# Kernel optimization log

Hardware: AMD Instinct MI355X
Metric: run time of the kernel (lower is better)

The kernel has to match this reference:

```python
import jax, jax.numpy as jnp
import numpy as np

HID = 1024   # hidden_dim
H = 16       # num_head
D = 64       # head_dim
W = 64       # window_size (one-sided attention radius)


def setup_inputs() -> dict:
    key = jax.random.key(0)
    ks = jax.random.split(key, 10)
    B, S = 2, 4096
    s = 0.02
    X = jax.random.normal(ks[0], (B, S, HID), jnp.float32)
    mask = jnp.ones((B, S), jnp.float32)
    Wq = jax.random.normal(ks[1], (HID, H * D), jnp.float32) * s
    bq = jnp.zeros((H * D,), jnp.float32)
    Wk = jax.random.normal(ks[2], (HID, H * D), jnp.float32) * s
    bk = jnp.zeros((H * D,), jnp.float32)
    Wv = jax.random.normal(ks[3], (HID, H * D), jnp.float32) * s
    bv = jnp.zeros((H * D,), jnp.float32)
    Wo = jax.random.normal(ks[4], (H * D, HID), jnp.float32) * s
    bo = jnp.zeros((HID,), jnp.float32)
    return dict(X=X, mask=mask, Wq=Wq, bq=bq, Wk=Wk, bk=bk, Wv=Wv, bv=bv, Wo=Wo, bo=bo)


def _chunk3(T, nC):
    # T: [B,H,S,D] -> [B,H,nC,3W,D]: for chunk c, keys of chunks c-1, c, c+1 (zero-padded at ends)
    B, Hh, S, Dd = T.shape
    Tp = jnp.pad(T, ((0, 0), (0, 0), (W, W), (0, 0))).reshape(B, Hh, nC + 2, W, Dd)
    return jnp.concatenate([Tp[:, :, :-2], Tp[:, :, 1:-1], Tp[:, :, 2:]], axis=3)


def reference(X, mask, Wq, bq, Wk, bk, Wv, bv, Wo, bo):
    B, S0, _ = X.shape
    pad = W - S0 % W  # matches torch: always >= 1 (full window if divisible)
    Xp = jnp.pad(X, ((0, 0), (0, pad), (0, 0)))
    mp = jnp.pad(mask, ((0, 0), (0, pad)))  # padded keys masked out
    S = S0 + pad
    nC = S // W

    def proj(Wm, b):
        return (Xp @ Wm + b).reshape(B, S, H, D).transpose(0, 2, 1, 3)  # [B,H,S,D]

    Q, K, V = proj(Wq, bq), proj(Wk, bk), proj(Wv, bv)
    Qc = Q.reshape(B, H, nC, W, D)
    K3 = _chunk3(K, nC)
    V3 = _chunk3(V, nC)

    # banded scores: query i attends keys j with |i - j| <= W
    scores = jnp.einsum('bhcqd,bhckd->bhcqk', Qc, K3) / jnp.asarray(np.sqrt(D), jnp.float32)
    qi = jnp.arange(W)[:, None]
    kj = jnp.arange(3 * W)[None, :]
    band = (kj >= qi) & (kj <= qi + 2 * W)  # [W, 3W]
    m3 = jnp.pad(mp, ((0, 0), (W, W))).reshape(B, nC + 2, W)
    m3 = jnp.concatenate([m3[:, :-2], m3[:, 1:-1], m3[:, 2:]], axis=2)  # [B,nC,3W]
    valid = band[None, None, None, :, :] & (m3[:, None, :, None, :] > 0)
    scores = jnp.where(valid, scores, -1e9)
    A = jax.nn.softmax(scores, axis=-1)
    ctx = jnp.einsum('bhcqk,bhckd->bhcqd', A, V3).reshape(B, H, S, D)
    out = ctx.transpose(0, 2, 1, 3).reshape(B, S, H * D) @ Wo + bo
    return out[:, :S0]
```

## Files before the change

kernel.cpp:

```cpp
#include <hip/hip_runtime.h>

typedef unsigned short u16;
typedef unsigned int u32;
typedef __bf16 bf16x8 __attribute__((ext_vector_type(8)));
typedef u16 u16x8 __attribute__((ext_vector_type(8)));
typedef float floatx4 __attribute__((ext_vector_type(4)));

#define MFMA16(a, b, c) __builtin_amdgcn_mfma_f32_16x16x32_bf16((a), (b), (c), 0, 0, 0)

#define B_ 2
#define S0 4096
#define NH 16
#define HD 64
#define HID 1024

__device__ __forceinline__ float bf2f(u16 u) {
  union { u32 i; float f; } x; x.i = ((u32)u) << 16; return x.f;
}
__device__ __forceinline__ u16 f2bf(float f) {
  union { float f; u32 i; } x; x.f = f;
  u32 r = x.i + 0x7FFFu + ((x.i >> 16) & 1u);
  return (u16)(r >> 16);
}

__device__ __forceinline__ void glds16(const u16* g, u16* l) {
  __builtin_amdgcn_global_load_lds(
      (const __attribute__((address_space(1))) u32*)g,
      (__attribute__((address_space(3))) u32*)l, 16, 0, 0);
}

__global__ __launch_bounds__(256) void prep(
    const float* __restrict__ X, const float* __restrict__ mask,
    const float* __restrict__ Wq, const float* __restrict__ bq,
    const float* __restrict__ Wk, const float* __restrict__ bk,
    const float* __restrict__ Wv, const float* __restrict__ bv,
    const float* __restrict__ Wo, const float* __restrict__ bo,
    u16* __restrict__ cX, u16* __restrict__ cmask, u16* __restrict__ cb,
    u16* __restrict__ WqkvT, u16* __restrict__ WoT) {
  __shared__ u16 tile[64][66];
  int bid = blockIdx.x;
  if (bid < 4096) {
    int i = (bid * 256 + threadIdx.x) * 8;
    const float4* Xv = (const float4*)(X + i);
    float4 a = Xv[0], b = Xv[1];
    u16x8 v;
    v[0] = f2bf(a.x); v[1] = f2bf(a.y); v[2] = f2bf(a.z); v[3] = f2bf(a.w);
    v[4] = f2bf(b.x); v[5] = f2bf(b.y); v[6] = f2bf(b.z); v[7] = f2bf(b.w);
    *(u16x8*)(cX + i) = v;
  } else if (bid < 4144) {
    int tid = (bid - 4096) * 256 + threadIdx.x;
    if (tid < B_ * S0) {
      cmask[tid] = f2bf(mask[tid]);
    } else {
      int j = tid - B_ * S0;
      int seg = j >> 10, idx = j & 1023;
      const float* src = (seg == 0) ? bq : (seg == 1) ? bk : (seg == 2) ? bv : bo;
      cb[seg * 1024 + idx] = f2bf(src[idx]);
    }
  } else {
    int idx = bid - 4144;
    int mat = idx >> 8;
    const float* src = (mat == 0) ? Wq : (mat == 1) ? Wk : (mat == 2) ? Wv : Wo;
    u16* dst = (mat < 3) ? (WqkvT + (size_t)mat * HID * HID) : WoT;
    int t0 = ((idx >> 4) & 15) * 64;
    int c0 = (idx & 15) * 64;
    int tx = threadIdx.x & 63, ty = threadIdx.x >> 6;
#pragma unroll
    for (int i = 0; i < 16; i++) {
      int r = i * 4 + ty;
      tile[r][tx] = f2bf(src[(size_t)(t0 + r) * HID + c0 + tx]);
    }
    __syncthreads();
#pragma unroll
    for (int i = 0; i < 16; i++) {
      int r = i * 4 + ty;
      dst[(size_t)(c0 + r) * HID + t0 + tx] = tile[tx][r];
    }
  }
}

template <int BN, int MODE, int NMAJOR, int SWZ>
__global__ __launch_bounds__(256) void gemm_bf16_tn(
    const u16* __restrict__ A, const u16* __restrict__ Bt,
    const u16* __restrict__ cb, void* __restrict__ outp, int K) {
  constexpr int NT = BN / 32;
  __shared__ alignas(16) u16 sA[128 * 64];
  __shared__ alignas(16) u16 sB[BN * 64];
  int t = threadIdx.x;
  int wave = t >> 6, lane = t & 63;
  int wm = wave >> 1, wn = wave & 1;
  int quad = lane >> 4, l16 = lane & 15;
  int tile_m, tile_n;
  if (SWZ) {
    int lin = blockIdx.y * gridDim.x + blockIdx.x;
    int wg = (lin & 7) * 256 + (lin >> 3);
    tile_m = (wg >> 5) * 128;
    tile_n = (wg & 31) * BN;
  } else {
    tile_m = (NMAJOR ? blockIdx.y : blockIdx.x) * 128;
    tile_n = (NMAJOR ? blockIdx.x : blockIdx.y) * BN;
  }

  floatx4 acc[4][NT] = {};

  int row_l = lane >> 3;
  int col_l = ((lane & 7) ^ row_l) * 8;
  const u16* Ag = A + (size_t)(tile_m + wave * 8 + row_l) * K + col_l;
  const u16* Bg = Bt + (size_t)(tile_n + wave * 8 + row_l) * K + col_l;
  u16* lA = sA + wave * 8 * 64;
  u16* lB = sB + wave * 8 * 64;

  for (int k0 = 0; k0 < K; k0 += 64) {
    __syncthreads();
#pragma unroll
    for (int r = 0; r < 4; r++)
      glds16(Ag + (size_t)(r * 32) * K + k0, lA + r * 2048);
#pragma unroll
    for (int r = 0; r < BN / 32; r++)
      glds16(Bg + (size_t)(r * 32) * K + k0, lB + r * 2048);
    __syncthreads();

#pragma unroll
    for (int ks = 0; ks < 2; ks++) {
      bf16x8 af[4], bfr[NT];
#pragma unroll
      for (int mt = 0; mt < 4; mt++) {
        int row = wm * 64 + mt * 16 + l16;
        int p = (ks * 4 + quad) ^ (row & 7);
        af[mt] = *(const bf16x8*)(sA + row * 64 + p * 8);
      }
#pragma unroll
      for (int nt = 0; nt < NT; nt++) {
        int row = wn * (BN / 2) + nt * 16 + l16;
        int p = (ks * 4 + quad) ^ (row & 7);
        bfr[nt] = *(const bf16x8*)(sB + row * 64 + p * 8);
      }
#pragma unroll
      for (int mt = 0; mt < 4; mt++)
#pragma unroll
        for (int nt = 0; nt < NT; nt++)
          acc[mt][nt] = MFMA16(af[mt], bfr[nt], acc[mt][nt]);
    }
  }

  if (MODE == 0) {
    u16* op = (u16*)outp;
#pragma unroll
    for (int mt = 0; mt < 4; mt++) {
      int row0 = tile_m + wm * 64 + mt * 16 + quad * 4;
      int bb = row0 >> 12;
      int sbase = row0 & (S0 - 1);
#pragma unroll
      for (int nt = 0; nt < NT; nt++) {
        int col = tile_n + wn * (BN / 2) + nt * 16 + l16;
        int p = col >> 10;
        int rem = col & 1023;
        float bias = bf2f(cb[p * 1024 + rem]);
        int hh = rem >> 6, dd = rem & 63;
        u16* dp = op + ((size_t)(((p * 2 + bb) * NH + hh)) * S0 + sbase) * HD + dd;
#pragma unroll
        for (int r = 0; r < 4; r++)
          dp[(size_t)r * HD] = f2bf(acc[mt][nt][r] + bias);
      }
    }
  } else {
    float* op = (float*)outp;
#pragma unroll
    for (int mt = 0; mt < 4; mt++) {
      int row0 = tile_m + wm * 64 + mt * 16 + quad * 4;
#pragma unroll
      for (int nt = 0; nt < NT; nt++) {
        int col = tile_n + wn * (BN / 2) + nt * 16 + l16;
        float bias = bf2f(cb[3 * 1024 + col]);
        float* dp = op + (size_t)row0 * HID + col;
#pragma unroll
        for (int r = 0; r < 4; r++)
          dp[(size_t)r * HID] = acc[mt][nt][r] + bias;
      }
    }
  }
}

__global__ __launch_bounds__(256) void attn_win(
    const u16* __restrict__ Q, const u16* __restrict__ Kp,
    const u16* __restrict__ Vp, const u16* __restrict__ cmask,
    u16* __restrict__ ctx) {
  __shared__ alignas(16) u16 buf0[208 * 64];
  __shared__ alignas(16) u16 sP[4 * 16 * 200];
  __shared__ u16 sMk[208];

  int lin = blockIdx.x;
  int bid = (lin & 7) * 256 + (lin >> 3);
  int c = bid & 63;
  int h = (bid >> 6) & 15;
  int b = bid >> 10;
  int t = threadIdx.x;
  int wave = t >> 6, lane = t & 63;
  int quad = lane >> 4, l16 = lane & 15;
  int koff = wave * 16;

  const u16* Qb = Q + (size_t)(b * NH + h) * S0 * HD;
  const u16* Kb = Kp + (size_t)(b * NH + h) * S0 * HD;
  const u16* Vb = Vp + (size_t)(b * NH + h) * S0 * HD;
  int kbase = (c - 1) * 64;

  int rrow = lane >> 3;
  int csrc = ((lane & 7) ^ rrow) * 8;
#pragma unroll
  for (int p = 0; p < 7; p++) {
    int sl0 = p * 32 + wave * 8;
    if (sl0 < 208) {
      int key = kbase + sl0 + rrow;
      int kc = key < 0 ? 0 : (key > S0 - 1 ? S0 - 1 : key);
      glds16(Kb + (size_t)kc * HD + csrc, buf0 + sl0 * 64);
    }
  }
  if (t < 208) {
    int j = kbase + t;
    sMk[t] = (j >= 0 && j < S0) ? cmask[(size_t)b * S0 + j] : (u16)0;
  }
  __syncthreads();

  floatx4 sc[9] = {};
  int qrow = c * 64 + wave * 16 + l16;
#pragma unroll
  for (int ks = 0; ks < 2; ks++) {
    bf16x8 aq = *(const bf16x8*)(Qb + (size_t)qrow * HD + ks * 32 + quad * 8);
#pragma unroll
    for (int nt = 0; nt < 9; nt++) {
      int slot = koff + nt * 16 + l16;
      int pch = ((ks * 4 + quad) ^ (l16 & 7)) * 8;
      bf16x8 bk = *(const bf16x8*)(buf0 + slot * 64 + pch);
      sc[nt] = MFMA16(aq, bk, sc[nt]);
    }
  }

  u16x8 vreg[7];
#pragma unroll
  for (int i = 0; i < 7; i++) {
    int e = i * 256 + t;
    if (e < 1664) {
      int dg = e / 208;
      int slot = e - dg * 208;
      int key = kbase + slot;
      int kc = key < 0 ? 0 : (key > S0 - 1 ? S0 - 1 : key);
      vreg[i] = *(const u16x8*)(Vb + (size_t)kc * HD + dg * 8);
    }
  }

  int qrel_base = wave * 16 + quad * 4;
  u16* myP = sP + wave * 16 * 200;
  float kmask[9];
#pragma unroll
  for (int nt = 0; nt < 9; nt++) kmask[nt] = bf2f(sMk[koff + nt * 16 + l16]);

#pragma unroll
  for (int reg = 0; reg < 4; reg++) {
    int qrel = qrel_base + reg;
    float v[9];
    float m = -3e38f;
#pragma unroll
    for (int nt = 0; nt < 9; nt++) {
      int slot = koff + nt * 16 + l16;
      bool ok = (slot >= qrel) && (slot <= qrel + 128) && (kmask[nt] > 0.f);
      float s = ok ? sc[nt][reg] * 0.125f : -1e30f;
      v[nt] = s;
      m = fmaxf(m, s);
    }
#pragma unroll
    for (int off = 1; off <= 8; off <<= 1) m = fmaxf(m, __shfl_xor(m, off));
    float sum = 0.f;
#pragma unroll
    for (int nt = 0; nt < 9; nt++) {
      float p = __expf(v[nt] - m);
      v[nt] = p;
      sum += p;
    }
#pragma unroll
    for (int off = 1; off <= 8; off <<= 1) sum += __shfl_xor(sum, off);
    float inv = 1.0f / sum;
    int prow = (quad * 4 + reg) * 200;
#pragma unroll
    for (int nt = 0; nt < 9; nt++)
      myP[prow + nt * 16 + l16] = f2bf(v[nt] * inv);
    myP[prow + 144 + l16] = 0;
  }
  __syncthreads();

#pragma unroll
  for (int i = 0; i < 7; i++) {
    int e = i * 256 + t;
    if (e < 1664) {
      int dg = e / 208;
      int slot = e - dg * 208;
#pragma unroll
      for (int j = 0; j < 8; j++) buf0[(dg * 8 + j) * 208 + slot] = vreg[i][j];
    }
  }
  __syncthreads();

  floatx4 oc[4] = {};
#pragma unroll
  for (int ks = 0; ks < 5; ks++) {
    bf16x8 ap = *(const bf16x8*)(myP + l16 * 200 + ks * 32 + quad * 8);
#pragma unroll
    for (int nt = 0; nt < 4; nt++) {
      bf16x8 bv =
          *(const bf16x8*)(buf0 + (nt * 16 + l16) * 208 + koff + ks * 32 + quad * 8);
      oc[nt] = MFMA16(ap, bv, oc[nt]);
    }
  }

  int srow = c * 64 + wave * 16 + quad * 4;
#pragma unroll
  for (int nt = 0; nt < 4; nt++) {
    u16* dp = ctx + (size_t)(b * S0 + srow) * HID + h * HD + nt * 16 + l16;
#pragma unroll
    for (int reg = 0; reg < 4; reg++)
      dp[(size_t)reg * HID] = f2bf(oc[nt][reg]);
  }
}

extern "C" void kernel_launch(void* const* d_in, const int* in_sizes, int n_in,
                              void* d_out, int out_size, void* d_ws, size_t ws_size,
                              hipStream_t stream) {
  const float* X = (const float*)d_in[0];
  const float* mask = (const float*)d_in[1];
  const float* Wq = (const float*)d_in[2];
  const float* bq = (const float*)d_in[3];
  const float* Wk = (const float*)d_in[4];
  const float* bk = (const float*)d_in[5];
  const float* Wv = (const float*)d_in[6];
  const float* bv = (const float*)d_in[7];
  const float* Wo = (const float*)d_in[8];
  const float* bo = (const float*)d_in[9];
  char* ws = (char*)d_ws;

  const size_t MB = 1048576;
  u16* cmask = (u16*)(ws + 256);
  u16* cb = (u16*)(ws + 256 + 16384);
  u16* cX = (u16*)(ws + 1 * MB);
  u16* WqkvT = (u16*)(ws + 17 * MB);
  u16* WoT = (u16*)(ws + 23 * MB);
  u16* QKV = (u16*)(ws + 25 * MB);
  u16* CTX = cX;

  const size_t per_qkv = (size_t)B_ * NH * S0 * HD;

  prep<<<4096 + 48 + 1024, 256, 0, stream>>>(X, mask, Wq, bq, Wk, bk, Wv, bv,
                                             Wo, bo, cX, cmask, cb, WqkvT, WoT);
  gemm_bf16_tn<96, 0, 1, 1><<<dim3(32, 64), 256, 0, stream>>>(cX, WqkvT, cb, QKV, HID);
  attn_win<<<dim3(B_ * NH * 64), 256, 0, stream>>>(QKV, QKV + per_qkv,
                                                   QKV + 2 * per_qkv, cmask, CTX);
  gemm_bf16_tn<128, 1, 0, 0><<<dim3(64, 8), 256, 0, stream>>>(CTX, WoT, cb, d_out, HID);
}
```

Measured before the change: 221.1 us.

## Process two adjacent query chunks per attention block to share K/V window loads

The windowed attention kernel now handles two consecutive 64-query chunks per block. It loads one shared K/V span of 256 to 272 keys instead of two separate 208-key spans, and the grid is halved. This removes the overlapping K/V and mask loads between neighbouring chunks. In exchange it uses more LDS per block (a wider V transpose buffer), which may lower occupancy, and it drops the previous block-index swizzle.

New measurement: 220.3 us. About the same (-0.4%).

```diff
diff --git a/kernel.cpp b/kernel.cpp
--- a/kernel.cpp
+++ b/kernel.cpp
@@ -13,6 +13,8 @@
 #define NH 16
 #define HD 64
 #define HID 1024
+#define VS 280
+#define PS 200
 
 __device__ __forceinline__ float bf2f(u16 u) {
   union { u32 i; float f; } x; x.i = ((u32)u) << 16; return x.f;
@@ -181,19 +183,17 @@
   }
 }
 
-__global__ __launch_bounds__(256) void attn_win(
+__global__ __launch_bounds__(256) void attn_win2(
     const u16* __restrict__ Q, const u16* __restrict__ Kp,
     const u16* __restrict__ Vp, const u16* __restrict__ cmask,
     u16* __restrict__ ctx) {
-  __shared__ alignas(16) u16 buf0[208 * 64];
-  __shared__ alignas(16) u16 sP[4 * 16 * 200];
-  __shared__ u16 sMk[208];
-
-  int lin = blockIdx.x;
-  int bid = (lin & 7) * 256 + (lin >> 3);
-  int c = bid & 63;
-  int h = (bid >> 6) & 15;
-  int b = bid >> 10;
+  __shared__ alignas(16) u16 buf0[64 * VS];
+  __shared__ alignas(16) u16 sP[4 * 16 * PS];
+  __shared__ u16 sMk[256];
+
+  int bid = blockIdx.x;
+  int cc = bid & 31, h = (bid >> 5) & 15, b = bid >> 9;
+  int c0 = cc * 2;
   int t = threadIdx.x;
   int wave = t >> 6, lane = t & 63;
   int quad = lane >> 4, l16 = lane & 15;
@@ -202,30 +202,28 @@
   const u16* Qb = Q + (size_t)(b * NH + h) * S0 * HD;
   const u16* Kb = Kp + (size_t)(b * NH + h) * S0 * HD;
   const u16* Vb = Vp + (size_t)(b * NH + h) * S0 * HD;
-  int kbase = (c - 1) * 64;
+  int kbase = (c0 - 1) * 64;
 
   int rrow = lane >> 3;
   int csrc = ((lane & 7) ^ rrow) * 8;
 #pragma unroll
-  for (int p = 0; p < 7; p++) {
+  for (int p = 0; p < 8; p++) {
     int sl0 = p * 32 + wave * 8;
-    if (sl0 < 208) {
-      int key = kbase + sl0 + rrow;
-      int kc = key < 0 ? 0 : (key > S0 - 1 ? S0 - 1 : key);
-      glds16(Kb + (size_t)kc * HD + csrc, buf0 + sl0 * 64);
-    }
-  }
-  if (t < 208) {
+    int key = kbase + sl0 + rrow;
+    int kc = key < 0 ? 0 : (key > S0 - 1 ? S0 - 1 : key);
+    glds16(Kb + (size_t)kc * HD + csrc, buf0 + sl0 * 64);
+  }
+  {
     int j = kbase + t;
     sMk[t] = (j >= 0 && j < S0) ? cmask[(size_t)b * S0 + j] : (u16)0;
   }
   __syncthreads();
 
   floatx4 sc[9] = {};
-  int qrow = c * 64 + wave * 16 + l16;
+  int qrowA = c0 * 64 + wave * 16 + l16;
 #pragma unroll
   for (int ks = 0; ks < 2; ks++) {
-    bf16x8 aq = *(const bf16x8*)(Qb + (size_t)qrow * HD + ks * 32 + quad * 8);
+    bf16x8 aq = *(const bf16x8*)(Qb + (size_t)qrowA * HD + ks * 32 + quad * 8);
 #pragma unroll
     for (int nt = 0; nt < 9; nt++) {
       int slot = koff + nt * 16 + l16;
@@ -235,90 +233,109 @@
     }
   }
 
-  u16x8 vreg[7];
-#pragma unroll
-  for (int i = 0; i < 7; i++) {
+  u16x8 vreg[9];
+#pragma unroll
+  for (int i = 0; i < 9; i++) {
     int e = i * 256 + t;
-    if (e < 1664) {
-      int dg = e / 208;
-      int slot = e - dg * 208;
+    if (e < 2176) {
+      int dg = e / 272;
+      int slot = e - dg * 272;
       int key = kbase + slot;
       int kc = key < 0 ? 0 : (key > S0 - 1 ? S0 - 1 : key);
       vreg[i] = *(const u16x8*)(Vb + (size_t)kc * HD + dg * 8);
     }
   }
 
-  int qrel_base = wave * 16 + quad * 4;
-  u16* myP = sP + wave * 16 * 200;
-  float kmask[9];
-#pragma unroll
-  for (int nt = 0; nt < 9; nt++) kmask[nt] = bf2f(sMk[koff + nt * 16 + l16]);
-
-#pragma unroll
-  for (int reg = 0; reg < 4; reg++) {
-    int qrel = qrel_base + reg;
-    float v[9];
-    float m = -3e38f;
+  u16* myP = sP + wave * 16 * PS;
+
+#define SOFTMAX_P(off)                                                       \
+  do {                                                                       \
+    float kmask[9];                                                          \
+    _Pragma("unroll") for (int nt = 0; nt < 9; nt++)                         \
+        kmask[nt] = bf2f(sMk[(off) + koff + nt * 16 + l16]);                 \
+    _Pragma("unroll") for (int reg = 0; reg < 4; reg++) {                    \
+      int qrel = (off) + wave * 16 + quad * 4 + reg;                         \
+      float v[9];                                                            \
+      float m = -3e38f;                                                      \
+      _Pragma("unroll") for (int nt = 0; nt < 9; nt++) {                     \
+        int slot = (off) + koff + nt * 16 + l16;                             \
+        bool ok = (slot >= qrel) && (slot <= qrel + 128) && (kmask[nt] > 0.f); \
+        float s = ok ? sc[nt][reg] * 0.125f : -1e30f;                        \
+        v[nt] = s;                                                           \
+        m = fmaxf(m, s);                                                     \
+      }                                                                      \
+      _Pragma("unroll") for (int o2 = 1; o2 <= 8; o2 <<= 1)                  \
+          m = fmaxf(m, __shfl_xor(m, o2));                                   \
+      float sum = 0.f;                                                       \
+      _Pragma("unroll") for (int nt = 0; nt < 9; nt++) {                     \
+        float pp = __expf(v[nt] - m);                                        \
+        v[nt] = pp;                                                          \
+        sum += pp;                                                           \
+      }                                                                      \
+      _Pragma("unroll") for (int o2 = 1; o2 <= 8; o2 <<= 1)                  \
+          sum += __shfl_xor(sum, o2);                                        \
+      float inv = 1.0f / sum;                                                \
+      int prow = (quad * 4 + reg) * PS;                                      \
+      _Pragma("unroll") for (int nt = 0; nt < 9; nt++)                       \
+          myP[prow + nt * 16 + l16] = f2bf(v[nt] * inv);                     \
+      myP[prow + 144 + l16] = 0;                                             \
+    }                                                                        \
+  } while (0)
+
+#define PV_CTX(off)                                                          \
+  do {                                                                       \
+    floatx4 oc[4] = {};                                                      \
+    _Pragma("unroll") for (int ks = 0; ks < 5; ks++) {                       \
+      bf16x8 ap = *(const bf16x8*)(myP + l16 * PS + ks * 32 + quad * 8);     \
+      _Pragma("unroll") for (int nt = 0; nt < 4; nt++) {                     \
+        bf16x8 bv = *(const bf16x8*)(buf0 + (nt * 16 + l16) * VS + (off) +   \
+                                     koff + ks * 32 + quad * 8);             \
+        oc[nt] = MFMA16(ap, bv, oc[nt]);                                     \
+      }                                                                      \
+    }                                                                        \
+    int srow = c0 * 64 + (off) + wave * 16 + quad * 4;                       \
+    _Pragma("unroll") for (int nt = 0; nt < 4; nt++) {                       \
+      u16* dp = ctx + (size_t)(b * S0 + srow) * HID + h * HD + nt * 16 + l16; \
+      _Pragma("unroll") for (int reg = 0; reg < 4; reg++)                    \
+          dp[(size_t)reg * HID] = f2bf(oc[nt][reg]);                         \
+    }                                                                        \
+  } while (0)
+
+  SOFTMAX_P(0);
+
+#pragma unroll
+  for (int nt = 0; nt < 9; nt++) sc[nt] = (floatx4){0.f, 0.f, 0.f, 0.f};
+  int qrowB = qrowA + 64;
+#pragma unroll
+  for (int ks = 0; ks < 2; ks++) {
+    bf16x8 aq = *(const bf16x8*)(Qb + (size_t)qrowB * HD + ks * 32 + quad * 8);
 #pragma unroll
     for (int nt = 0; nt < 9; nt++) {
-      int slot = koff + nt * 16 + l16;
-      bool ok = (slot >= qrel) && (slot <= qrel + 128) && (kmask[nt] > 0.f);
-      float s = ok ? sc[nt][reg] * 0.125f : -1e30f;
-      v[nt] = s;
-      m = fmaxf(m, s);
-    }
-#pragma unroll
-    for (int off = 1; off <= 8; off <<= 1) m = fmaxf(m, __shfl_xor(m, off));
-    float sum = 0.f;
-#pragma unroll
-    for (int nt = 0; nt < 9; nt++) {
-      float p = __expf(v[nt] - m);
-      v[nt] = p;
-      sum += p;
-    }
-#pragma unroll
-    for (int off = 1; off <= 8; off <<= 1) sum += __shfl_xor(sum, off);
-    float inv = 1.0f / sum;
-    int prow = (quad * 4 + reg) * 200;
-#pragma unroll
-    for (int nt = 0; nt < 9; nt++)
-      myP[prow + nt * 16 + l16] = f2bf(v[nt] * inv);
-    myP[prow + 144 + l16] = 0;
+      int slot = 64 + koff + nt * 16 + l16;
+      int pch = ((ks * 4 + quad) ^ (l16 & 7)) * 8;
+      bf16x8 bk = *(const bf16x8*)(buf0 + slot * 64 + pch);
+      sc[nt] = MFMA16(aq, bk, sc[nt]);
+    }
   }
   __syncthreads();
 
 #pragma unroll
-  for (int i = 0; i < 7; i++) {
+  for (int i = 0; i < 9; i++) {
     int e = i * 256 + t;
-    if (e < 1664) {
-      int dg = e / 208;
-      int slot = e - dg * 208;
-#pragma unroll
-      for (int j = 0; j < 8; j++) buf0[(dg * 8 + j) * 208 + slot] = vreg[i][j];
+    if (e < 2176) {
+      int dg = e / 272;
+      int slot = e - dg * 272;
+#pragma unroll
+      for (int j = 0; j < 8; j++) buf0[(dg * 8 + j) * VS + slot] = vreg[i][j];
     }
   }
   __syncthreads();
 
-  floatx4 oc[4] = {};
-#pragma unroll
-  for (int ks = 0; ks < 5; ks++) {
-    bf16x8 ap = *(const bf16x8*)(myP + l16 * 200 + ks * 32 + quad * 8);
-#pragma unroll
-    for (int nt = 0; nt < 4; nt++) {
-      bf16x8 bv =
-          *(const bf16x8*)(buf0 + (nt * 16 + l16) * 208 + koff + ks * 32 + quad * 8);
-      oc[nt] = MFMA16(ap, bv, oc[nt]);
-    }
-  }
-
-  int srow = c * 64 + wave * 16 + quad * 4;
-#pragma unroll
-  for (int nt = 0; nt < 4; nt++) {
-    u16* dp = ctx + (size_t)(b * S0 + srow) * HID + h * HD + nt * 16 + l16;
-#pragma unroll
-    for (int reg = 0; reg < 4; reg++)
-      dp[(size_t)reg * HID] = f2bf(oc[nt][reg]);
-  }
+  PV_CTX(0);
+  SOFTMAX_P(64);
+  PV_CTX(64);
+#undef SOFTMAX_P
+#undef PV_CTX
 }
 
 extern "C" void kernel_launch(void* const* d_in, const int* in_sizes, int n_in,
@@ -350,7 +367,7 @@
   prep<<<4096 + 48 + 1024, 256, 0, stream>>>(X, mask, Wq, bq, Wk, bk, Wv, bv,
                                              Wo, bo, cX, cmask, cb, WqkvT, WoT);
   gemm_bf16_tn<96, 0, 1, 1><<<dim3(32, 64), 256, 0, stream>>>(cX, WqkvT, cb, QKV, HID);
-  attn_win<<<dim3(B_ * NH * 64), 256, 0, stream>>>(QKV, QKV + per_qkv,
-                                                   QKV + 2 * per_qkv, cmask, CTX);
+  attn_win2<<<dim3(B_ * NH * 32), 256, 0, stream>>>(QKV, QKV + per_qkv,
+                                                    QKV + 2 * per_qkv, cmask, CTX);
   gemm_bf16_tn<128, 1, 0, 0><<<dim3(64, 8), 256, 0, stream>>>(CTX, WoT, cb, d_out, HID);
 }
```
